# Optimization experiments

Hardware: AMD Instinct MI355X
Metric: run time of the kernel (lower is better)

## Reference

```python
import jax, jax.numpy as jnp
import numpy as np
from jax import lax

B, T, H, L = 1024, 512, 64, 3


def setup_inputs() -> dict:
    key = jax.random.key(0)
    ks = jax.random.split(key, 7)
    s = 1.0 / np.sqrt(H)  # pytorch default init scale (uniform bound); randn*s is fine for a numeric reference
    return {
        "x": jax.random.normal(ks[0], (B, T, H), dtype=jnp.float32),
        "W_ih": jax.random.normal(ks[1], (L, H, H), dtype=jnp.float32) * s,
        "W_hh": jax.random.normal(ks[2], (L, H, H), dtype=jnp.float32) * s,
        "b_ih": jax.random.normal(ks[3], (L, H), dtype=jnp.float32) * s,
        "b_hh": jax.random.normal(ks[4], (L, H), dtype=jnp.float32) * s,
        "fc_w": jax.random.normal(ks[5], (1, H), dtype=jnp.float32) * s,
        "fc_b": jax.random.normal(ks[6], (1,), dtype=jnp.float32) * s,
    }


def _run_layer(x_seq, Wih, Whh, bih, bhh):
    # x_seq: [B, T, Hin]; precompute the input projection once (parallel over T)
    xproj = jnp.einsum("bti,hi->bth", x_seq, Wih) + bih  # [B, T, H]

    def step(h, xt):
        h = jnp.tanh(xt + h @ Whh.T + bhh)
        return h, h

    h0 = jnp.zeros((x_seq.shape[0], Whh.shape[0]), dtype=x_seq.dtype)
    _, ys = lax.scan(step, h0, jnp.swapaxes(xproj, 0, 1))  # scan over time
    return jnp.swapaxes(ys, 0, 1)  # [B, T, H]


def reference(x, W_ih, W_hh, b_ih, b_hh, fc_w, fc_b):
    h = x
    for l in range(L):  # small fixed layer count
        h = _run_layer(h, W_ih[l], W_hh[l], b_ih[l], b_hh[l])
    # fc applied to last timestep only
    return h[:, -1, :] @ fc_w.T + fc_b  # [B, 1]
```

## Files before the change

### kernel.cpp

```cpp
#include <hip/hip_runtime.h>


typedef __attribute__((ext_vector_type(2))) float f32x2;
typedef __attribute__((ext_vector_type(4))) float f32x4;

#define RNN_B 1024
#define RNN_T 512
#define RNN_H 64
#define RNN_L 3
#define RPB   2

static __device__ __forceinline__ f32x2 mk2(float a, float b) {
    f32x2 r; r.x = a; r.y = b; return r;
}

__global__ __launch_bounds__(RNN_L * 64)
__attribute__((amdgpu_waves_per_eu(2, 2)))
void rnn_pipeline(const float* __restrict__ x,
                  const float* __restrict__ Wih,
                  const float* __restrict__ Whh,
                  const float* __restrict__ bih,
                  const float* __restrict__ bhh,
                  const float* __restrict__ fcw,
                  const float* __restrict__ fcb,
                  float* __restrict__ out)
{
    __shared__ f32x4 ring[RNN_L + 1][2][RPB][RNN_H / 4];

    const int lane = threadIdx.x & 63;
    const int l    = threadIdx.x >> 6;
    const int b0   = blockIdx.x * RPB;

    f32x2 wi[RNN_H / 2], wh[RNN_H / 2];
    {
        const f32x4* wr = (const f32x4*)(Wih + ((size_t)l * RNN_H + lane) * RNN_H);
        const f32x4* hr = (const f32x4*)(Whh + ((size_t)l * RNN_H + lane) * RNN_H);
#pragma unroll
        for (int c = 0; c < RNN_H / 4; ++c) {
            f32x4 a = wr[c];
            wi[2*c+0] = mk2(a.x, a.y); wi[2*c+1] = mk2(a.z, a.w);
            f32x4 d = hr[c];
            wh[2*c+0] = mk2(d.x, d.y); wh[2*c+1] = mk2(d.z, d.w);
        }
    }
#pragma unroll
    for (int i = 0; i < RNN_H / 2; ++i)
        asm volatile("" : "+v"(wi[i]), "+v"(wh[i]));

    const float bias = bih[l * RNN_H + lane] + bhh[l * RNN_H + lane];
    const float fw   = fcw[lane];
    const float fb   = fcb[0];

#pragma unroll
    for (int sl = 0; sl < 2; ++sl)
#pragma unroll
        for (int r = 0; r < RPB; ++r)
            ((float*)&ring[l][sl][r][0])[lane] = 0.0f;

    const float* xb = x + (size_t)b0 * RNN_T * RNN_H;
    const size_t rowstride = (size_t)RNN_T * RNN_H;
    float xr0 = 0.f, xn0 = 0.f, xr1 = 0.f, xn1 = 0.f;
    if (l == 0) {
        ((float*)&ring[3][0][0][0])[lane] = xb[lane];
        ((float*)&ring[3][0][1][0])[lane] = xb[rowstride + lane];
        xr0 = xb[RNN_H + lane];                 xn0 = xb[2 * RNN_H + lane];
        xr1 = xb[rowstride + RNN_H + lane];     xn1 = xb[rowstride + 2 * RNN_H + lane];
    }
    __syncthreads();

    const int in_ring = (l == 0) ? 3 : (l - 1);
    float hv0 = 0.0f, hv1 = 0.0f;

    for (int s = 0; s < RNN_T + RNN_L - 1; ++s) {
        const int t = s - l;
        const bool active = (t >= 0) && (t < RNN_T);
        if (active) {
            const int si = t & 1;
            const int sh = (t - 1) & 1;

            f32x2 a00 = mk2(bias, 0.f), a01 = mk2(0.f, 0.f);
            f32x2 a02 = mk2(0.f, 0.f),  a03 = mk2(0.f, 0.f);
            f32x2 a10 = mk2(bias, 0.f), a11 = mk2(0.f, 0.f);
            f32x2 a12 = mk2(0.f, 0.f),  a13 = mk2(0.f, 0.f);

#pragma unroll
            for (int c = 0; c < RNN_H / 4; ++c) {
                f32x4 v0 = ring[in_ring][si][0][c];
                f32x4 v1 = ring[in_ring][si][1][c];
                a00 += mk2(v0.x, v0.y) * wi[2*c+0];
                a01 += mk2(v0.z, v0.w) * wi[2*c+1];
                a10 += mk2(v1.x, v1.y) * wi[2*c+0];
                a11 += mk2(v1.z, v1.w) * wi[2*c+1];
            }
#pragma unroll
            for (int c = 0; c < RNN_H / 4; ++c) {
                f32x4 u0 = ring[l][sh][0][c];
                f32x4 u1 = ring[l][sh][1][c];
                a02 += mk2(u0.x, u0.y) * wh[2*c+0];
                a03 += mk2(u0.z, u0.w) * wh[2*c+1];
                a12 += mk2(u1.x, u1.y) * wh[2*c+0];
                a13 += mk2(u1.z, u1.w) * wh[2*c+1];
            }
            const f32x2 s0 = (a00 + a02) + (a01 + a03);
            const f32x2 s1 = (a10 + a12) + (a11 + a13);
            const float pre0 = s0.x + s0.y;
            const float pre1 = s1.x + s1.y;

            const float ax0 = fabsf(pre0);
            const float e0  = __expf(-2.0f * ax0);
            hv0 = copysignf((1.0f - e0) / (1.0f + e0), pre0);
            const float ax1 = fabsf(pre1);
            const float e1  = __expf(-2.0f * ax1);
            hv1 = copysignf((1.0f - e1) / (1.0f + e1), pre1);

            ((float*)&ring[l][t & 1][0][0])[lane] = hv0;
            ((float*)&ring[l][t & 1][1][0])[lane] = hv1;

            if (l == 0) {
                if (t + 1 < RNN_T) {
                    ((float*)&ring[3][(t + 1) & 1][0][0])[lane] = xr0;
                    ((float*)&ring[3][(t + 1) & 1][1][0])[lane] = xr1;
                }
                xr0 = xn0; xr1 = xn1;
                const int tn = (t + 3 < RNN_T) ? (t + 3) : (RNN_T - 1);
                xn0 = xb[(size_t)tn * RNN_H + lane];
                xn1 = xb[rowstride + (size_t)tn * RNN_H + lane];
            }

            if (l == 2 && t == RNN_T - 1) {
                float p0 = hv0 * fw, p1 = hv1 * fw;
#pragma unroll
                for (int off = 32; off > 0; off >>= 1) {
                    p0 += __shfl_xor(p0, off, 64);
                    p1 += __shfl_xor(p1, off, 64);
                }
                if (lane == 0) {
                    out[b0 + 0] = p0 + fb;
                    out[b0 + 1] = p1 + fb;
                }
            }
        }
        __syncthreads();
    }
}

extern "C" void kernel_launch(void* const* d_in, const int* in_sizes, int n_in,
                              void* d_out, int out_size, void* d_ws, size_t ws_size,
                              hipStream_t stream)
{
    const float* x   = (const float*)d_in[0];
    const float* Wih = (const float*)d_in[1];
    const float* Whh = (const float*)d_in[2];
    const float* bih = (const float*)d_in[3];
    const float* bhh = (const float*)d_in[4];
    const float* fcw = (const float*)d_in[5];
    const float* fcb = (const float*)d_in[6];
    float* out = (float*)d_out;

    rnn_pipeline<<<dim3(RNN_B / RPB), dim3(RNN_L * 64), 0, stream>>>(
        x, Wih, Whh, bih, bhh, fcw, fcb, out);
}
```

Measured before the change: 958.0 us.

## Split each layer into input-projection and recurrent waves in a deeper pipeline

Each layer now uses two waves instead of one. One wave computes the input projection W_ih·x_t and writes it to a shared buffer, and the other wave computes the recurrent W_hh·h_{t-1} product, adds the projection and bias, and applies tanh. This halves the dependent FMA chain on each pipeline step and halves per-wave weight registers, at the cost of twice as many waves, extra LDS traffic, and a pipeline that is longer by three steps. The __syncthreads is also replaced with a raw lgkmcnt wait plus s_barrier, and the x prefetch is one step deeper.

```diff
diff --git a/kernel.cpp b/kernel.cpp
--- a/kernel.cpp
+++ b/kernel.cpp
@@ -9,13 +9,15 @@
 #define RNN_H 64
 #define RNN_L 3
 #define RPB   2
+#define NW    (2 * RNN_L)
+#define STEPS (RNN_T + NW - 1)
 
 static __device__ __forceinline__ f32x2 mk2(float a, float b) {
     f32x2 r; r.x = a; r.y = b; return r;
 }
 
-__global__ __launch_bounds__(RNN_L * 64)
-__attribute__((amdgpu_waves_per_eu(2, 2)))
+__global__ __launch_bounds__(NW * 64)
+__attribute__((amdgpu_waves_per_eu(3, 3)))
 void rnn_pipeline(const float* __restrict__ x,
                   const float* __restrict__ Wih,
                   const float* __restrict__ Whh,
@@ -25,122 +27,137 @@
                   const float* __restrict__ fcb,
                   float* __restrict__ out)
 {
-    __shared__ f32x4 ring[RNN_L + 1][2][RPB][RNN_H / 4];
+    __shared__ f32x4 xring[2][RPB][RNN_H / 4];
+    __shared__ f32x4 hring[RNN_L][2][RPB][RNN_H / 4];
+    __shared__ float xcring[RNN_L][2][RPB][RNN_H];
 
     const int lane = threadIdx.x & 63;
-    const int l    = threadIdx.x >> 6;
+    const int w    = threadIdx.x >> 6;
+    const int l    = w >> 1;
+    const int isA  = !(w & 1);
     const int b0   = blockIdx.x * RPB;
 
-    f32x2 wi[RNN_H / 2], wh[RNN_H / 2];
+    f32x2 wt[RNN_H / 2];
     {
-        const f32x4* wr = (const f32x4*)(Wih + ((size_t)l * RNN_H + lane) * RNN_H);
-        const f32x4* hr = (const f32x4*)(Whh + ((size_t)l * RNN_H + lane) * RNN_H);
+        const float* Wsrc = isA ? (Wih + ((size_t)l * RNN_H + lane) * RNN_H)
+                                : (Whh + ((size_t)l * RNN_H + lane) * RNN_H);
+        const f32x4* wr = (const f32x4*)Wsrc;
 #pragma unroll
         for (int c = 0; c < RNN_H / 4; ++c) {
             f32x4 a = wr[c];
-            wi[2*c+0] = mk2(a.x, a.y); wi[2*c+1] = mk2(a.z, a.w);
-            f32x4 d = hr[c];
-            wh[2*c+0] = mk2(d.x, d.y); wh[2*c+1] = mk2(d.z, d.w);
+            wt[2*c+0] = mk2(a.x, a.y);
+            wt[2*c+1] = mk2(a.z, a.w);
         }
     }
 #pragma unroll
     for (int i = 0; i < RNN_H / 2; ++i)
-        asm volatile("" : "+v"(wi[i]), "+v"(wh[i]));
+        asm volatile("" : "+v"(wt[i]));
 
     const float bias = bih[l * RNN_H + lane] + bhh[l * RNN_H + lane];
     const float fw   = fcw[lane];
     const float fb   = fcb[0];
 
+    if (w < RNN_L) {
 #pragma unroll
-    for (int sl = 0; sl < 2; ++sl)
+        for (int sl = 0; sl < 2; ++sl)
 #pragma unroll
-        for (int r = 0; r < RPB; ++r)
-            ((float*)&ring[l][sl][r][0])[lane] = 0.0f;
+            for (int r = 0; r < RPB; ++r)
+                ((float*)&hring[w][sl][r][0])[lane] = 0.0f;
+    }
 
     const float* xb = x + (size_t)b0 * RNN_T * RNN_H;
-    const size_t rowstride = (size_t)RNN_T * RNN_H;
-    float xr0 = 0.f, xn0 = 0.f, xr1 = 0.f, xn1 = 0.f;
-    if (l == 0) {
-        ((float*)&ring[3][0][0][0])[lane] = xb[lane];
-        ((float*)&ring[3][0][1][0])[lane] = xb[rowstride + lane];
-        xr0 = xb[RNN_H + lane];                 xn0 = xb[2 * RNN_H + lane];
-        xr1 = xb[rowstride + RNN_H + lane];     xn1 = xb[rowstride + 2 * RNN_H + lane];
+    const size_t rs = (size_t)RNN_T * RNN_H;
+    float xr0 = 0.f, xr1 = 0.f, xn10 = 0.f, xn11 = 0.f, xn20 = 0.f, xn21 = 0.f;
+    if (w == 0) {
+        ((float*)&xring[0][0][0])[lane] = xb[lane];
+        ((float*)&xring[0][1][0])[lane] = xb[rs + lane];
+        xr0  = xb[1 * RNN_H + lane];  xr1  = xb[rs + 1 * RNN_H + lane];
+        xn10 = xb[2 * RNN_H + lane];  xn11 = xb[rs + 2 * RNN_H + lane];
+        xn20 = xb[3 * RNN_H + lane];  xn21 = xb[rs + 3 * RNN_H + lane];
     }
     __syncthreads();
 
-    const int in_ring = (l == 0) ? 3 : (l - 1);
     float hv0 = 0.0f, hv1 = 0.0f;
 
-    for (int s = 0; s < RNN_T + RNN_L - 1; ++s) {
-        const int t = s - l;
+    for (int s = 0; s < STEPS; ++s) {
+        const int t = s - w;
         const bool active = (t >= 0) && (t < RNN_T);
         if (active) {
             const int si = t & 1;
-            const int sh = (t - 1) & 1;
+            if (isA) {
+                const f32x4* in0 = (l == 0) ? &xring[si][0][0]
+                                            : &hring[l - 1][si][0][0];
+                const f32x4* in1 = (l == 0) ? &xring[si][1][0]
+                                            : &hring[l - 1][si][1][0];
+                f32x2 a00 = mk2(0.f, 0.f), a01 = mk2(0.f, 0.f);
+                f32x2 a10 = mk2(0.f, 0.f), a11 = mk2(0.f, 0.f);
+#pragma unroll
+                for (int c = 0; c < RNN_H / 4; ++c) {
+                    f32x4 v0 = in0[c];
+                    f32x4 v1 = in1[c];
+                    a00 += mk2(v0.x, v0.y) * wt[2*c+0];
+                    a01 += mk2(v0.z, v0.w) * wt[2*c+1];
+                    a10 += mk2(v1.x, v1.y) * wt[2*c+0];
+                    a11 += mk2(v1.z, v1.w) * wt[2*c+1];
+                }
+                const f32x2 s0 = a00 + a01, s1 = a10 + a11;
+                xcring[l][si][0][lane] = s0.x + s0.y;
+                xcring[l][si][1][lane] = s1.x + s1.y;
 
-            f32x2 a00 = mk2(bias, 0.f), a01 = mk2(0.f, 0.f);
-            f32x2 a02 = mk2(0.f, 0.f),  a03 = mk2(0.f, 0.f);
-            f32x2 a10 = mk2(bias, 0.f), a11 = mk2(0.f, 0.f);
-            f32x2 a12 = mk2(0.f, 0.f),  a13 = mk2(0.f, 0.f);
+                if (w == 0) {
+                    if (t + 1 < RNN_T) {
+                        ((float*)&xring[(t + 1) & 1][0][0])[lane] = xr0;
+                        ((float*)&xring[(t + 1) & 1][1][0])[lane] = xr1;
+                    }
+                    xr0 = xn10; xr1 = xn11;
+                    xn10 = xn20; xn11 = xn21;
+                    const int tn = (t + 4 < RNN_T) ? (t + 4) : (RNN_T - 1);
+                    xn20 = xb[(size_t)tn * RNN_H + lane];
+                    xn21 = xb[rs + (size_t)tn * RNN_H + lane];
+                }
+            } else {
+                const int sh = (t - 1) & 1;
+                f32x2 a00 = mk2(0.f, 0.f), a01 = mk2(0.f, 0.f);
+                f32x2 a10 = mk2(0.f, 0.f), a11 = mk2(0.f, 0.f);
+#pragma unroll
+                for (int c = 0; c < RNN_H / 4; ++c) {
+                    f32x4 u0 = hring[l][sh][0][c];
+                    f32x4 u1 = hring[l][sh][1][c];
+                    a00 += mk2(u0.x, u0.y) * wt[2*c+0];
+                    a01 += mk2(u0.z, u0.w) * wt[2*c+1];
+                    a10 += mk2(u1.x, u1.y) * wt[2*c+0];
+                    a11 += mk2(u1.z, u1.w) * wt[2*c+1];
+                }
+                const f32x2 s0 = a00 + a01, s1 = a10 + a11;
+                const float pre0 = s0.x + s0.y + bias + xcring[l][si][0][lane];
+                const float pre1 = s1.x + s1.y + bias + xcring[l][si][1][lane];
 
+                const float ax0 = fabsf(pre0);
+                const float e0  = __expf(-2.0f * ax0);
+                hv0 = copysignf((1.0f - e0) / (1.0f + e0), pre0);
+                const float ax1 = fabsf(pre1);
+                const float e1  = __expf(-2.0f * ax1);
+                hv1 = copysignf((1.0f - e1) / (1.0f + e1), pre1);
+
+                ((float*)&hring[l][si][0][0])[lane] = hv0;
+                ((float*)&hring[l][si][1][0])[lane] = hv1;
+
+                if (w == NW - 1 && t == RNN_T - 1) {
+                    float p0 = hv0 * fw, p1 = hv1 * fw;
 #pragma unroll
-            for (int c = 0; c < RNN_H / 4; ++c) {
-                f32x4 v0 = ring[in_ring][si][0][c];
-                f32x4 v1 = ring[in_ring][si][1][c];
-                a00 += mk2(v0.x, v0.y) * wi[2*c+0];
-                a01 += mk2(v0.z, v0.w) * wi[2*c+1];
-                a10 += mk2(v1.x, v1.y) * wi[2*c+0];
-                a11 += mk2(v1.z, v1.w) * wi[2*c+1];
-            }
-#pragma unroll
-            for (int c = 0; c < RNN_H / 4; ++c) {
-                f32x4 u0 = ring[l][sh][0][c];
-                f32x4 u1 = ring[l][sh][1][c];
-                a02 += mk2(u0.x, u0.y) * wh[2*c+0];
-                a03 += mk2(u0.z, u0.w) * wh[2*c+1];
-                a12 += mk2(u1.x, u1.y) * wh[2*c+0];
-                a13 += mk2(u1.z, u1.w) * wh[2*c+1];
-            }
-            const f32x2 s0 = (a00 + a02) + (a01 + a03);
-            const f32x2 s1 = (a10 + a12) + (a11 + a13);
-            const float pre0 = s0.x + s0.y;
-            const float pre1 = s1.x + s1.y;
-
-            const float ax0 = fabsf(pre0);
-            const float e0  = __expf(-2.0f * ax0);
-            hv0 = copysignf((1.0f - e0) / (1.0f + e0), pre0);
-            const float ax1 = fabsf(pre1);
-            const float e1  = __expf(-2.0f * ax1);
-            hv1 = copysignf((1.0f - e1) / (1.0f + e1), pre1);
-
-            ((float*)&ring[l][t & 1][0][0])[lane] = hv0;
-            ((float*)&ring[l][t & 1][1][0])[lane] = hv1;
-
-            if (l == 0) {
-                if (t + 1 < RNN_T) {
-                    ((float*)&ring[3][(t + 1) & 1][0][0])[lane] = xr0;
-                    ((float*)&ring[3][(t + 1) & 1][1][0])[lane] = xr1;
-                }
-                xr0 = xn0; xr1 = xn1;
-                const int tn = (t + 3 < RNN_T) ? (t + 3) : (RNN_T - 1);
-                xn0 = xb[(size_t)tn * RNN_H + lane];
-                xn1 = xb[rowstride + (size_t)tn * RNN_H + lane];
-            }
-
-            if (l == 2 && t == RNN_T - 1) {
-                float p0 = hv0 * fw, p1 = hv1 * fw;
-#pragma unroll
-                for (int off = 32; off > 0; off >>= 1) {
-                    p0 += __shfl_xor(p0, off, 64);
-                    p1 += __shfl_xor(p1, off, 64);
-                }
-                if (lane == 0) {
-                    out[b0 + 0] = p0 + fb;
-                    out[b0 + 1] = p1 + fb;
+                    for (int off = 32; off > 0; off >>= 1) {
+                        p0 += __shfl_xor(p0, off, 64);
+                        p1 += __shfl_xor(p1, off, 64);
+                    }
+                    if (lane == 0) {
+                        out[b0 + 0] = p0 + fb;
+                        out[b0 + 1] = p1 + fb;
+                    }
                 }
             }
         }
-        __syncthreads();
+        asm volatile("s_waitcnt lgkmcnt(0)" ::: "memory");
+        __builtin_amdgcn_s_barrier();
     }
 }
 
@@ -157,6 +174,6 @@
     const float* fcb = (const float*)d_in[6];
     float* out = (float*)d_out;
 
-    rnn_pipeline<<<dim3(RNN_B / RPB), dim3(RNN_L * 64), 0, stream>>>(
+    rnn_pipeline<<<dim3(RNN_B / RPB), dim3(NW * 64), 0, stream>>>(
         x, Wih, Whh, bih, bhh, fcw, fcb, out);
 }
```

Result: slower. 1.135 ms (+18.5%).
